# Kernel optimization log

Hardware: AMD Instinct MI355X
Metric: run time of the kernel (lower is better)

## Reference

```python
import jax, jax.numpy as jnp
import numpy as np

D_MODEL = 1024
N_HEADS = 16  # long-term branch; short/medium use N_HEADS // 2


def _band_bias(seq_len, scale_factor):
    # Intended semantics of create_temporal_mask: position i may attend to
    # positions j >= i - scale_factor (recent past + all future); positions
    # further than scale_factor in the past are blocked.
    i = jnp.arange(seq_len)[:, None]
    j = jnp.arange(seq_len)[None, :]
    return jnp.where(j >= i - scale_factor, 0.0, -1e9).astype(jnp.float32)


def _mha(x, w_in, b_in, w_out, b_out, n_heads, bias):
    # Faithful nn.MultiheadAttention (batch_first, eval/no dropout).
    B, S, D = x.shape
    dk = D // n_heads
    qkv = x @ w_in.T + b_in                       # [B,S,3D]
    q, k, v = jnp.split(qkv, 3, axis=-1)
    def heads(t):
        return t.reshape(B, S, n_heads, dk).transpose(0, 2, 1, 3)  # [B,H,S,dk]
    q, k, v = heads(q), heads(k), heads(v)
    scores = jnp.einsum('bhid,bhjd->bhij', q, k) / np.sqrt(dk).astype(np.float32)
    if bias is not None:
        scores = scores + bias
    attn = jax.nn.softmax(scores, axis=-1)        # [B,H,S,S]
    out = jnp.einsum('bhij,bhjd->bhid', attn, v)  # [B,H,S,dk]
    out = out.transpose(0, 2, 1, 3).reshape(B, S, D)
    return out @ w_out.T + b_out, attn


def _layernorm(x, gamma, beta, eps=1e-5):
    mu = jnp.mean(x, axis=-1, keepdims=True)
    var = jnp.var(x, axis=-1, keepdims=True)
    return (x - mu) * jax.lax.rsqrt(var + eps) * gamma + beta


def setup_inputs() -> dict:
    key = jax.random.key(0)
    ks = jax.random.split(key, 12)
    D = D_MODEL
    s = 0.02
    inp = {
        'x': jax.random.normal(ks[0], (2, 2048, D), dtype=jnp.float32),
        'w_in_s': jax.random.normal(ks[1], (3 * D, D), dtype=jnp.float32) * s,
        'b_in_s': jnp.zeros((3 * D,), dtype=jnp.float32),
        'wo_s': jax.random.normal(ks[2], (D, D), dtype=jnp.float32) * s,
        'bo_s': jnp.zeros((D,), dtype=jnp.float32),
        'w_in_m': jax.random.normal(ks[3], (3 * D, D), dtype=jnp.float32) * s,
        'b_in_m': jnp.zeros((3 * D,), dtype=jnp.float32),
        'wo_m': jax.random.normal(ks[4], (D, D), dtype=jnp.float32) * s,
        'bo_m': jnp.zeros((D,), dtype=jnp.float32),
        'w_in_l': jax.random.normal(ks[5], (3 * D, D), dtype=jnp.float32) * s,
        'b_in_l': jnp.zeros((3 * D,), dtype=jnp.float32),
        'wo_l': jax.random.normal(ks[6], (D, D), dtype=jnp.float32) * s,
        'bo_l': jnp.zeros((D,), dtype=jnp.float32),
        'w_comb': jax.random.normal(ks[7], (D, 3 * D), dtype=jnp.float32) * s,
        'b_comb': jnp.zeros((D,), dtype=jnp.float32),
        'gamma': jnp.ones((D,), dtype=jnp.float32),
        'beta': jnp.zeros((D,), dtype=jnp.float32),
    }
    return inp


def reference(x, w_in_s, b_in_s, wo_s, bo_s,
              w_in_m, b_in_m, wo_m, bo_m,
              w_in_l, b_in_l, wo_l, bo_l,
              w_comb, b_comb, gamma, beta):
    B, S, D = x.shape
    short_bias = _band_bias(S, 10)
    medium_bias = _band_bias(S, 30)
    short_out, _ = _mha(x, w_in_s, b_in_s, wo_s, bo_s, N_HEADS // 2, short_bias)
    medium_out, _ = _mha(x, w_in_m, b_in_m, wo_m, bo_m, N_HEADS // 2, medium_bias)
    long_out, attn = _mha(x, w_in_l, b_in_l, wo_l, bo_l, N_HEADS, None)
    attn_weights = jnp.mean(attn, axis=1)  # torch default average_attn_weights=True -> [B,S,S]
    combined = jnp.concatenate([short_out, medium_out, long_out], axis=-1)
    output = combined @ w_comb.T + b_comb
    return _layernorm(output + x, gamma, beta), attn_weights
```

## Files before the change

### kernel.cpp

```cpp
#include <hip/hip_runtime.h>
#include <hip/hip_bf16.h>
#include <math.h>

#define B_ 2
#define S_ 2048
#define D_ 1024
#define M_ (B_*S_)
#define CTXLD 3072

typedef _Float16 half8_t __attribute__((ext_vector_type(8)));
typedef _Float16 half4_t __attribute__((ext_vector_type(4)));
typedef float    f32x4  __attribute__((ext_vector_type(4)));

#define GL2LDS(g, l) __builtin_amdgcn_global_load_lds( \
    (const __attribute__((address_space(1))) void*)(uintptr_t)(g), \
    (__attribute__((address_space(3))) void*)(l), 16, 0, 0)

struct GemmBatch {
    const _Float16* A;
    const _Float16* W;
    const float*    bias;
    void*           C;
    void*           C2;
};

template<int MODE, bool SWZ>
__global__ __launch_bounds__(256) void gemm_f16(
    GemmBatch b0, GemmBatch b1, GemmBatch b2, int lda, int ldw, int ldc, int K)
{
    __shared__ __align__(16) _Float16 As[2*128*32];
    __shared__ __align__(16) _Float16 Bs[2*128*32];

    int bx, by, bz;
    if (SWZ) {
        const int gx = gridDim.x, gy = gridDim.y;
        const int total = gx * gy * gridDim.z;
        const int lin = blockIdx.x + gx * (blockIdx.y + gy * blockIdx.z);
        const int lbid = (lin & 7) * (total >> 3) + (lin >> 3);
        bx = lbid % gx;
        const int rem = lbid / gx;
        by = rem % gy;
        bz = rem / gy;
    } else {
        bx = blockIdx.x; by = blockIdx.y; bz = blockIdx.z;
    }

    const GemmBatch G = (bz == 0) ? b0 : ((bz == 1) ? b1 : b2);

    const int t = threadIdx.x, lane = t & 63, w = t >> 6;
    const int bm = bx * 128, bn = by * 128;
    const int wm = (w >> 1) * 64, wn = (w & 1) * 64;
    const int fr = lane & 15, q8 = (lane >> 4) * 8;
    const int srow = lane >> 2, scol = (lane & 3) * 8;

    f32x4 acc[4][4] = {};

    const _Float16* Ab = G.A + (size_t)(bm + w*32 + srow) * lda + scol;
    const _Float16* Wb = G.W + (size_t)(bn + w*32 + srow) * ldw + scol;

    for (int k0 = 0; k0 < K; k0 += 64) {
        __syncthreads();
        #pragma unroll
        for (int kc = 0; kc < 2; kc++)
            #pragma unroll
            for (int ii = 0; ii < 2; ii++) {
                GL2LDS(Ab + (size_t)(ii*16)*lda + k0 + kc*32,
                       As + kc*4096 + w*1024 + ii*512);
                GL2LDS(Wb + (size_t)(ii*16)*ldw + k0 + kc*32,
                       Bs + kc*4096 + w*1024 + ii*512);
            }
        __syncthreads();
        #pragma unroll
        for (int kc = 0; kc < 2; kc++) {
            half8_t af[4], bf[4];
            #pragma unroll
            for (int mt = 0; mt < 4; mt++)
                af[mt] = *(const half8_t*)&As[kc*4096 + (wm + mt*16 + fr)*32 + q8];
            #pragma unroll
            for (int nt = 0; nt < 4; nt++)
                bf[nt] = *(const half8_t*)&Bs[kc*4096 + (wn + nt*16 + fr)*32 + q8];
            #pragma unroll
            for (int mt = 0; mt < 4; mt++)
                #pragma unroll
                for (int nt = 0; nt < 4; nt++)
                    acc[mt][nt] = __builtin_amdgcn_mfma_f32_16x16x32_f16(
                        af[mt], bf[nt], acc[mt][nt], 0, 0, 0);
        }
    }

    const int cl = lane & 15;
    const int rq = (lane >> 4) * 4;

    if (MODE == 2 && bn >= 2048) {
        #pragma unroll
        for (int mt = 0; mt < 4; mt++) {
            int row0 = bm + wm + mt*16 + rq;
            #pragma unroll
            for (int nt = 0; nt < 4; nt++) {
                int gcol = bn + wn + nt*16 + cl;
                float bv = G.bias[gcol];
                half4_t hv = {(_Float16)(acc[mt][nt][0] + bv),
                              (_Float16)(acc[mt][nt][1] + bv),
                              (_Float16)(acc[mt][nt][2] + bv),
                              (_Float16)(acc[mt][nt][3] + bv)};
                *(half4_t*)((_Float16*)G.C2 + (size_t)(gcol - 2048) * M_ + row0) = hv;
            }
        }
        return;
    }

    #pragma unroll
    for (int mt = 0; mt < 4; mt++) {
        #pragma unroll
        for (int r = 0; r < 4; r++) {
            size_t grow = (size_t)(bm + wm + mt*16 + rq + r);
            #pragma unroll
            for (int nt = 0; nt < 4; nt++) {
                int gcol = bn + wn + nt*16 + cl;
                float v = acc[mt][nt][r] + ((MODE == 3) ? 0.f : G.bias[gcol]);
                if (MODE == 0)
                    ((float*)G.C)[grow * ldc + gcol] = v;
                else
                    ((_Float16*)G.C)[grow * ldc + gcol] = (_Float16)v;
            }
        }
    }
}

struct CastArgs {
    const float* s[5];
    _Float16*    d[5];
    int          nb[5];
};

__global__ __launch_bounds__(256) void cast_all(CastArgs a)
{
    int off = blockIdx.x;
    int seg = 0;
    while (seg < 4 && off >= a.nb[seg]) { off -= a.nb[seg]; seg++; }
    int i = off * 256 + threadIdx.x;
    float4 v = ((const float4*)a.s[seg])[i];
    half4_t h = {(_Float16)v.x, (_Float16)v.y, (_Float16)v.z, (_Float16)v.w};
    ((half4_t*)a.d[seg])[i] = h;
}

__global__ __launch_bounds__(256) void transpose_cast_wo(
    const float* s0, const float* s1, const float* s2,
    _Float16* d0, _Float16* d1, _Float16* d2)
{
    __shared__ float T[64][68];
    const float* src = blockIdx.z == 0 ? s0 : (blockIdx.z == 1 ? s1 : s2);
    _Float16*    dst = blockIdx.z == 0 ? d0 : (blockIdx.z == 1 ? d1 : d2);
    const int db = blockIdx.x * 64;
    const int eb = blockIdx.y * 64;
    const int r = threadIdx.x >> 4;
    const int c = (threadIdx.x & 15) * 4;

    #pragma unroll
    for (int rr = 0; rr < 4; rr++) {
        float4 v = *(const float4*)&src[(size_t)(db + rr*16 + r)*1024 + eb + c];
        T[rr*16 + r][c+0] = v.x; T[rr*16 + r][c+1] = v.y;
        T[rr*16 + r][c+2] = v.z; T[rr*16 + r][c+3] = v.w;
    }
    __syncthreads();
    #pragma unroll
    for (int rr = 0; rr < 4; rr++) {
        int e = rr*16 + r;
        half4_t hv = {(_Float16)T[c+0][e], (_Float16)T[c+1][e],
                      (_Float16)T[c+2][e], (_Float16)T[c+3][e]};
        *(half4_t*)&dst[(size_t)(eb + e)*1024 + db + c] = hv;
    }
}

__global__ __launch_bounds__(256) void beff_kernel(
    const float* __restrict__ w_comb, const float* __restrict__ b_comb,
    const float* __restrict__ bo_s, const float* __restrict__ bo_m,
    const float* __restrict__ bo_l, float* __restrict__ beff)
{
    __shared__ float red[4];
    const int n = blockIdx.x, t = threadIdx.x;
    float s = 0.f;
    for (int d = t; d < 1024; d += 256)
        s += w_comb[(size_t)n*3072 + d]        * bo_s[d]
           + w_comb[(size_t)n*3072 + 1024 + d] * bo_m[d]
           + w_comb[(size_t)n*3072 + 2048 + d] * bo_l[d];
    #pragma unroll
    for (int m = 32; m >= 1; m >>= 1) s += __shfl_xor(s, m);
    if ((t & 63) == 0) red[t >> 6] = s;
    __syncthreads();
    if (t == 0) beff[n] = b_comb[n] + red[0] + red[1] + red[2] + red[3];
}

template<int DK, int BJ, bool LOUT>
__device__ __forceinline__ void flash_body(
    _Float16* lds, float* Lw,
    const _Float16* __restrict__ qk, const _Float16* __restrict__ vT,
    _Float16* __restrict__ ctx, float* __restrict__ lout,
    int window, int b, int h, int qblk, int H)
{
    constexpr int KS  = DK / 32;
    constexpr int DT  = DK / 16;
    constexpr int JT  = BJ / 16;
    constexpr int JC  = BJ / 32;
    constexpr int LDP = 40;

    _Float16* Ks = lds;
    _Float16* Vs = lds + DK*BJ;
    _Float16* Ps = lds + 2*DK*BJ;

    const int t = threadIdx.x, lane = t & 63, w = t >> 6;
    const int fr = lane & 15, g = lane >> 4, k8 = g * 8;
    const int k8s = (g ^ ((fr >> 1) & 3)) * 8;
    const int blkQ = qblk * 64;
    const int qlo  = blkQ + w * 16;

    const float sc = ((DK == 128) ? 0.08838834764831845f : 0.125f) * 1.44269504f;

    _Float16* PsW = Ps + w * 16 * LDP;
    const int srow = lane >> 2;
    const int ssw  = ((lane & 3) ^ ((srow >> 1) & 3)) * 8;

    half8_t qf[KS];
    #pragma unroll
    for (int kk = 0; kk < KS; kk++)
        qf[kk] = *(const half8_t*)&qk[(size_t)(b*S_ + qlo + fr)*2048 + h*DK + kk*32 + k8];

    f32x4 O[DT] = {};
    float lsum = 0.f;

    for (int j0 = 0; j0 < S_; j0 += BJ) {
        if (window >= 0 && j0 + BJ - 1 < blkQ - window) continue;
        __syncthreads();

        #pragma unroll
        for (int kk = 0; kk < KS; kk++)
            #pragma unroll
            for (int ii = 0; ii < BJ/64; ii++)
                GL2LDS(&qk[(size_t)(b*S_ + j0 + w*(BJ/4) + ii*16 + srow)*2048
                           + 1024 + h*DK + kk*32 + ssw],
                       &Ks[kk*BJ*32 + w*(BJ/4)*32 + ii*512]);
        #pragma unroll
        for (int jc = 0; jc < JC; jc++)
            #pragma unroll
            for (int ii = 0; ii < DK/64; ii++)
                GL2LDS(&vT[(size_t)(h*DK + w*(DK/4) + ii*16 + srow)*M_
                           + b*S_ + j0 + jc*32 + ssw],
                       &Vs[jc*DK*32 + w*(DK/4)*32 + ii*512]);
        __syncthreads();

        f32x4 st[JT];
        #pragma unroll
        for (int jt = 0; jt < JT; jt++) {
            f32x4 s = {};
            #pragma unroll
            for (int kk = 0; kk < KS; kk++) {
                half8_t kf = *(const half8_t*)&Ks[kk*BJ*32 + (jt*16 + fr)*32 + k8s];
                s = __builtin_amdgcn_mfma_f32_16x16x32_f16(kf, qf[kk], s, 0, 0, 0);
            }
            st[jt] = s;
        }

        const bool full = (window < 0) || (j0 >= qlo + 15 - window);
        #pragma unroll
        for (int kc = 0; kc < JC; kc++) {
            #pragma unroll
            for (int jh = 0; jh < 2; jh++) {
                int jt = kc*2 + jh;
                float p[4];
                #pragma unroll
                for (int r = 0; r < 4; r++) {
                    float pv = exp2f(st[jt][r] * sc);
                    if (!full) {
                        int jg = j0 + jt*16 + g*4 + r;
                        if (jg < (qlo + fr) - window) pv = 0.f;
                    }
                    p[r] = pv;
                    lsum += pv;
                }
                half4_t ph = {(_Float16)p[0], (_Float16)p[1],
                              (_Float16)p[2], (_Float16)p[3]};
                *(half4_t*)&PsW[fr*LDP + jh*16 + g*4] = ph;
            }
            half8_t pf = *(const half8_t*)&PsW[fr*LDP + k8];
            #pragma unroll
            for (int dt = 0; dt < DT; dt++) {
                half8_t vf = *(const half8_t*)&Vs[kc*DK*32 + (dt*16 + fr)*32 + k8s];
                O[dt] = __builtin_amdgcn_mfma_f32_16x16x32_f16(pf, vf, O[dt], 0, 0, 0);
            }
        }
    }

    lsum += __shfl_xor(lsum, 16);
    lsum += __shfl_xor(lsum, 32);
    if (g == 0) Lw[w*16 + fr] = lsum;
    float linv[4];
    #pragma unroll
    for (int r = 0; r < 4; r++)
        linv[r] = 1.f / Lw[w*16 + g*4 + r];

    if (LOUT && g == 0)
        lout[(size_t)(b*H + h)*S_ + qlo + fr] = lsum;

    #pragma unroll
    for (int r = 0; r < 4; r++) {
        _Float16* cp = ctx + (size_t)(b*S_ + qlo + g*4 + r)*CTXLD + h*DK;
        #pragma unroll
        for (int dt = 0; dt < DT; dt++)
            cp[dt*16 + fr] = (_Float16)(O[dt][r] * linv[r]);
    }
}

__global__ __launch_bounds__(256, 4) void flash_mega(
    const _Float16* __restrict__ qk_s, const _Float16* __restrict__ qk_m,
    const _Float16* __restrict__ qk_l,
    const _Float16* __restrict__ vT_s, const _Float16* __restrict__ vT_m,
    const _Float16* __restrict__ vT_l,
    _Float16* __restrict__ ctxall, float* __restrict__ lbuf)
{
    __shared__ __align__(16) _Float16 lds[18944];
    __shared__ float Lw[64];

    const int hwb = blockIdx.x;
    const int bid = (hwb & 7) * 256 + (hwb >> 3);
    if (bid < 1024) {
        int qblk = bid & 31, h = (bid >> 5) & 15, b = bid >> 9;
        flash_body<64, 128, true>(lds, Lw, qk_l, vT_l, ctxall + 2048, lbuf,
                                  -1, b, h, qblk, 16);
    } else {
        int r = bid - 1024;
        int qblk = r & 31;
        int h = (r >> 5) & 7;
        int z = r >> 8;
        int br = z >> 1, b = z & 1;
        flash_body<128, 64, false>(lds, Lw, br ? qk_m : qk_s, br ? vT_m : vT_s,
                                   ctxall + (br ? 1024 : 0), nullptr,
                                   br ? 30 : 10, b, h, qblk, 8);
    }
}

__global__ __launch_bounds__(256, 4) void attn_mean3(
    const _Float16* __restrict__ qk,
    const float* __restrict__ lbuf,
    float* __restrict__ attn)
{
    __shared__ __align__(16) _Float16 Ks[2 * 2 * 128 * 32];

    const int t = threadIdx.x, lane = t & 63, w = t >> 6;
    const int fr = lane & 15, g = lane >> 4, k8 = g * 8;
    const int k8s = (g ^ ((fr >> 1) & 3)) * 8;
    const int j0 = blockIdx.x * 128;
    const int irow = blockIdx.y * 64 + w * 16;
    const int b = blockIdx.z;
    const float c1 = 0.125f * 1.44269504f;
    const int srow = lane >> 2;
    const int ssw  = ((lane & 3) ^ ((srow >> 1) & 3)) * 8;

    f32x4 acc[8] = {};

    for (int hp = 0; hp < 16; hp += 2) {
        __syncthreads();
        #pragma unroll
        for (int hh = 0; hh < 2; hh++)
            #pragma unroll
            for (int kk = 0; kk < 2; kk++)
                #pragma unroll
                for (int ii = 0; ii < 2; ii++)
                    GL2LDS(&qk[(size_t)(b*S_ + j0 + w*32 + ii*16 + srow)*2048
                               + 1024 + (hp+hh)*64 + kk*32 + ssw],
                           &Ks[hh*8192 + kk*4096 + w*1024 + ii*512]);
        __syncthreads();

        #pragma unroll
        for (int hh = 0; hh < 2; hh++) {
            const int h = hp + hh;
            half8_t af[2];
            #pragma unroll
            for (int kk = 0; kk < 2; kk++)
                af[kk] = *(const half8_t*)
                    &qk[(size_t)(b*S_ + irow + fr)*2048 + h*64 + kk*32 + k8];

            float lg[4];
            #pragma unroll
            for (int r = 0; r < 4; r++)
                lg[r] = __log2f(lbuf[(size_t)(b*16 + h)*S_ + irow + g*4 + r]) + 4.0f;

            #pragma unroll
            for (int nt = 0; nt < 8; nt++) {
                f32x4 s = {};
                #pragma unroll
                for (int kk = 0; kk < 2; kk++) {
                    half8_t bf = *(const half8_t*)
                        &Ks[hh*8192 + kk*4096 + (nt*16 + fr)*32 + k8s];
                    s = __builtin_amdgcn_mfma_f32_16x16x32_f16(af[kk], bf, s, 0, 0, 0);
                }
                #pragma unroll
                for (int r = 0; r < 4; r++)
                    acc[nt][r] += exp2f(s[r] * c1 - lg[r]);
            }
        }
    }

    #pragma unroll
    for (int r = 0; r < 4; r++) {
        float* p = attn + (size_t)(b*S_ + irow + g*4 + r)*S_ + j0;
        #pragma unroll
        for (int nt = 0; nt < 8; nt++)
            p[nt*16 + fr] = acc[nt][r];
    }
}

__global__ __launch_bounds__(256) void ln_residual(
    const float* __restrict__ pre, const float* __restrict__ x,
    const float* __restrict__ gamma, const float* __restrict__ beta,
    float* __restrict__ out)
{
    __shared__ float redS[4], redQ[4];
    const int row = blockIdx.x;
    const int t = threadIdx.x;
    size_t base = (size_t)row * D_ + t * 4;

    float4 v  = *(const float4*)(pre + base);
    float4 xv = *(const float4*)(x + base);
    v.x += xv.x; v.y += xv.y; v.z += xv.z; v.w += xv.w;

    float s = v.x + v.y + v.z + v.w;
    float q = v.x*v.x + v.y*v.y + v.z*v.z + v.w*v.w;
    #pragma unroll
    for (int m = 32; m >= 1; m >>= 1) {
        s += __shfl_xor(s, m);
        q += __shfl_xor(q, m);
    }
    int wave = t >> 6;
    if ((t & 63) == 0) { redS[wave] = s; redQ[wave] = q; }
    __syncthreads();
    s = redS[0] + redS[1] + redS[2] + redS[3];
    q = redQ[0] + redQ[1] + redQ[2] + redQ[3];

    float mean = s * (1.f / D_);
    float var  = q * (1.f / D_) - mean * mean;
    float rstd = rsqrtf(var + 1e-5f);

    float4 g  = *(const float4*)(gamma + t * 4);
    float4 be = *(const float4*)(beta + t * 4);
    float4 o;
    o.x = (v.x - mean) * rstd * g.x + be.x;
    o.y = (v.y - mean) * rstd * g.y + be.y;
    o.z = (v.z - mean) * rstd * g.z + be.z;
    o.w = (v.w - mean) * rstd * g.w + be.w;
    *(float4*)(out + base) = o;
}

extern "C" void kernel_launch(void* const* d_in, const int* in_sizes, int n_in,
                              void* d_out, int out_size, void* d_ws, size_t ws_size,
                              hipStream_t stream)
{
    (void)in_sizes; (void)n_in; (void)out_size; (void)ws_size;
    const float* x      = (const float*)d_in[0];
    const float* w_in_s = (const float*)d_in[1];
    const float* b_in_s = (const float*)d_in[2];
    const float* wo_s   = (const float*)d_in[3];
    const float* bo_s   = (const float*)d_in[4];
    const float* w_in_m = (const float*)d_in[5];
    const float* b_in_m = (const float*)d_in[6];
    const float* wo_m   = (const float*)d_in[7];
    const float* bo_m   = (const float*)d_in[8];
    const float* w_in_l = (const float*)d_in[9];
    const float* b_in_l = (const float*)d_in[10];
    const float* wo_l   = (const float*)d_in[11];
    const float* bo_l   = (const float*)d_in[12];
    const float* w_comb = (const float*)d_in[13];
    const float* b_comb = (const float*)d_in[14];
    const float* gamma  = (const float*)d_in[15];
    const float* beta   = (const float*)d_in[16];

    float* out    = (float*)d_out;
    float* attn_o = out + (size_t)M_ * D_;

    char* W = (char*)d_ws;
    _Float16* w_in_s_h = (_Float16*)(W);
    _Float16* w_in_m_h = (_Float16*)(W + 6291456);
    _Float16* w_in_l_h = (_Float16*)(W + 12582912);
    _Float16* w_comb_h = (_Float16*)(W + 18874368);
    _Float16* woT_s    = (_Float16*)(W + 25165824);
    _Float16* woT_m    = (_Float16*)(W + 27262976);
    _Float16* woT_l    = (_Float16*)(W + 29360128);
    _Float16* weff     = (_Float16*)(W + 31457280);
    _Float16* qk_s     = (_Float16*)(W + 37748736);
    _Float16* qk_m     = (_Float16*)(W + 54525952);
    _Float16* qk_l     = (_Float16*)(W + 71303168);
    _Float16* vT_s     = (_Float16*)(W + 88080384);
    _Float16* vT_m     = (_Float16*)(W + 96468992);
    _Float16* ctxall   = (_Float16*)(W + 104857600);
    _Float16* x_h      = (_Float16*)(W + 130023424);
    float*    lbuf     = (float*)   (W + 138412032);
    float*    beff     = (float*)   (W + 138674432);
    _Float16* vT_l     = w_comb_h;
    float*    pre      = (float*)qk_m;

    dim3 blk(256);
    GemmBatch nil = { nullptr, nullptr, nullptr, nullptr, nullptr };

    CastArgs ca;
    ca.s[0]=x;      ca.d[0]=x_h;      ca.nb[0]=4096;
    ca.s[1]=w_in_s; ca.d[1]=w_in_s_h; ca.nb[1]=3072;
    ca.s[2]=w_in_m; ca.d[2]=w_in_m_h; ca.nb[2]=3072;
    ca.s[3]=w_in_l; ca.d[3]=w_in_l_h; ca.nb[3]=3072;
    ca.s[4]=w_comb; ca.d[4]=w_comb_h; ca.nb[4]=3072;
    cast_all<<<dim3(16384), blk, 0, stream>>>(ca);

    transpose_cast_wo<<<dim3(16, 16, 3), blk, 0, stream>>>(
        wo_s, wo_m, wo_l, woT_s, woT_m, woT_l);

    GemmBatch we0 = { w_comb_h + 0,    woT_s, nullptr, weff + 0,    nullptr };
    GemmBatch we1 = { w_comb_h + 1024, woT_m, nullptr, weff + 1024, nullptr };
    GemmBatch we2 = { w_comb_h + 2048, woT_l, nullptr, weff + 2048, nullptr };
    gemm_f16<3, false><<<dim3(8, 8, 3), blk, 0, stream>>>(we0, we1, we2, 3072, 1024, 3072, 1024);

    beff_kernel<<<dim3(1024), blk, 0, stream>>>(w_comb, b_comb, bo_s, bo_m, bo_l, beff);

    GemmBatch qs = { x_h, w_in_s_h, b_in_s, qk_s, vT_s };
    GemmBatch qm = { x_h, w_in_m_h, b_in_m, qk_m, vT_m };
    GemmBatch ql = { x_h, w_in_l_h, b_in_l, qk_l, vT_l };
    gemm_f16<2, true><<<dim3(M_/128, 3072/128, 3), blk, 0, stream>>>(qs, qm, ql, D_, D_, 2048, D_);

    flash_mega<<<dim3(2048), blk, 0, stream>>>(
        qk_s, qk_m, qk_l, vT_s, vT_m, vT_l, ctxall, lbuf);

    attn_mean3<<<dim3(S_/128, S_/64, B_), blk, 0, stream>>>(qk_l, lbuf, attn_o);

    GemmBatch fb = { ctxall, weff, beff, pre, nullptr };
    gemm_f16<0, false><<<dim3(M_/128, D_/128, 1), blk, 0, stream>>>(fb, nil, nil, 3072, 3072, D_, 3072);

    ln_residual<<<dim3(M_), blk, 0, stream>>>(pre, x, gamma, beta, out);
}
```

Measured before the change: 567.7 us.

## Double-buffer K/V tiles in flash attention kernel and start windowed loops late

The flash attention body now keeps two LDS buffers for K and V. The async global-to-LDS load of the next tile is issued while the current tile is computed, so load latency overlaps with MFMA work. The windowed branches compute their first useful key block directly instead of skipping blocks with continue. The extra LDS roughly doubles per-block shared memory and lowers launch bounds from 4 to 2 blocks per CU, reducing occupancy. The QKV GEMM template flag is also switched from true to false.

Result: no change. 572.0 us (+0.8%).

```diff
diff --git a/kernel.cpp b/kernel.cpp
--- a/kernel.cpp
+++ b/kernel.cpp
@@ -198,15 +198,14 @@
     _Float16* __restrict__ ctx, float* __restrict__ lout,
     int window, int b, int h, int qblk, int H)
 {
-    constexpr int KS  = DK / 32;
-    constexpr int DT  = DK / 16;
-    constexpr int JT  = BJ / 16;
-    constexpr int JC  = BJ / 32;
-    constexpr int LDP = 40;
-
-    _Float16* Ks = lds;
-    _Float16* Vs = lds + DK*BJ;
-    _Float16* Ps = lds + 2*DK*BJ;
+    constexpr int KS   = DK / 32;
+    constexpr int DT   = DK / 16;
+    constexpr int JT   = BJ / 16;
+    constexpr int JC   = BJ / 32;
+    constexpr int LDP  = 40;
+    constexpr int KVSZ = 2 * DK * BJ;
+
+    _Float16* Ps = lds + 2 * KVSZ;
 
     const int t = threadIdx.x, lane = t & 63, w = t >> 6;
     const int fr = lane & 15, g = lane >> 4, k8 = g * 8;
@@ -228,25 +227,40 @@
     f32x4 O[DT] = {};
     float lsum = 0.f;
 
-    for (int j0 = 0; j0 < S_; j0 += BJ) {
-        if (window >= 0 && j0 + BJ - 1 < blkQ - window) continue;
-        __syncthreads();
-
+    int jstart = 0;
+    if (window >= 0) {
+        int lo = blkQ - window - BJ + 1;
+        if (lo > 0) jstart = ((lo + BJ - 1) / BJ) * BJ;
+    }
+
+    auto stage = [&](int j0, int buf) {
+        _Float16* Kb = lds + buf * KVSZ;
+        _Float16* Vb = Kb + DK * BJ;
         #pragma unroll
         for (int kk = 0; kk < KS; kk++)
             #pragma unroll
             for (int ii = 0; ii < BJ/64; ii++)
                 GL2LDS(&qk[(size_t)(b*S_ + j0 + w*(BJ/4) + ii*16 + srow)*2048
                            + 1024 + h*DK + kk*32 + ssw],
-                       &Ks[kk*BJ*32 + w*(BJ/4)*32 + ii*512]);
+                       &Kb[kk*BJ*32 + w*(BJ/4)*32 + ii*512]);
         #pragma unroll
         for (int jc = 0; jc < JC; jc++)
             #pragma unroll
             for (int ii = 0; ii < DK/64; ii++)
                 GL2LDS(&vT[(size_t)(h*DK + w*(DK/4) + ii*16 + srow)*M_
                            + b*S_ + j0 + jc*32 + ssw],
-                       &Vs[jc*DK*32 + w*(DK/4)*32 + ii*512]);
+                       &Vb[jc*DK*32 + w*(DK/4)*32 + ii*512]);
+    };
+
+    stage(jstart, 0);
+    int cur = 0;
+
+    for (int j0 = jstart; j0 < S_; j0 += BJ) {
         __syncthreads();
+        if (j0 + BJ < S_) stage(j0 + BJ, cur ^ 1);
+
+        _Float16* Ks = lds + cur * KVSZ;
+        _Float16* Vs = Ks + DK * BJ;
 
         f32x4 st[JT];
         #pragma unroll
@@ -288,6 +302,7 @@
                 O[dt] = __builtin_amdgcn_mfma_f32_16x16x32_f16(pf, vf, O[dt], 0, 0, 0);
             }
         }
+        cur ^= 1;
     }
 
     lsum += __shfl_xor(lsum, 16);
@@ -310,14 +325,14 @@
     }
 }
 
-__global__ __launch_bounds__(256, 4) void flash_mega(
+__global__ __launch_bounds__(256, 2) void flash_mega(
     const _Float16* __restrict__ qk_s, const _Float16* __restrict__ qk_m,
     const _Float16* __restrict__ qk_l,
     const _Float16* __restrict__ vT_s, const _Float16* __restrict__ vT_m,
     const _Float16* __restrict__ vT_l,
     _Float16* __restrict__ ctxall, float* __restrict__ lbuf)
 {
-    __shared__ __align__(16) _Float16 lds[18944];
+    __shared__ __align__(16) _Float16 lds[35328];
     __shared__ float Lw[64];
 
     const int hwb = blockIdx.x;
@@ -521,7 +536,7 @@
     GemmBatch qs = { x_h, w_in_s_h, b_in_s, qk_s, vT_s };
     GemmBatch qm = { x_h, w_in_m_h, b_in_m, qk_m, vT_m };
     GemmBatch ql = { x_h, w_in_l_h, b_in_l, qk_l, vT_l };
-    gemm_f16<2, true><<<dim3(M_/128, 3072/128, 3), blk, 0, stream>>>(qs, qm, ql, D_, D_, 2048, D_);
+    gemm_f16<2, false><<<dim3(M_/128, 3072/128, 3), blk, 0, stream>>>(qs, qm, ql, D_, D_, 2048, D_);
 
     flash_mega<<<dim3(2048), blk, 0, stream>>>(
         qk_s, qk_m, qk_l, vT_s, vT_m, vT_l, ctxall, lbuf);
```
